# Optimization experiments

Measured on AMD Instinct MI355X. Metric: run time of the kernel, lower is better.

Reference implementation:

```python
import jax, jax.numpy as jnp
import numpy as np

EMBED = 1024
D_FF = 4 * EMBED
N_EXPERTS = 8
TOP_K = 2
B, S = 2, 1024


def setup_inputs() -> dict:
    key = jax.random.key(0)
    ks = jax.random.split(key, 10)
    sc_d = 1.0 / np.sqrt(EMBED)
    sc_h = 1.0 / np.sqrt(D_FF)
    return {
        "inputs": jax.random.normal(ks[0], (B, S, EMBED), jnp.float32),
        # router MLP: Linear(D,4D) -> ReLU -> Linear(4D,E)
        "rw1": jax.random.normal(ks[1], (EMBED, D_FF), jnp.float32) * sc_d,
        "rb1": jnp.zeros((D_FF,), jnp.float32),
        "rw2": jax.random.normal(ks[2], (D_FF, N_EXPERTS), jnp.float32) * sc_h,
        "rb2": jnp.zeros((N_EXPERTS,), jnp.float32),
        # stacked expert weights: Linear(D,4D) -> ReLU -> Linear(4D,D)
        "W1": jax.random.normal(ks[3], (N_EXPERTS, EMBED, D_FF), jnp.float32) * sc_d,
        "b1": jnp.zeros((N_EXPERTS, D_FF), jnp.float32),
        "W2": jax.random.normal(ks[4], (N_EXPERTS, D_FF, EMBED), jnp.float32) * sc_h,
        "b2": jnp.zeros((N_EXPERTS, EMBED), jnp.float32),
    }


def reference(inputs, rw1, rb1, rw2, rb2, W1, b1, W2, b2):
    Bb, Ss, D = inputs.shape
    T = Bb * Ss
    xf = inputs.reshape(T, D)  # [T, D]

    # Router: scores over experts, keep top-k, softmax over kept entries only.
    score = jax.nn.relu(xf @ rw1 + rb1) @ rw2 + rb2          # [T, E]
    _, topi = jax.lax.top_k(score, TOP_K)                    # [T, K]
    mask = jnp.zeros(score.shape, bool).at[jnp.arange(T)[:, None], topi].set(True)
    gate = jax.nn.softmax(jnp.where(mask, score, -jnp.inf), axis=-1)  # [T, E]

    # Dense per-expert MLP weighted by gate; gate==0 for non-top-k experts,
    # matching the original masked gather/scatter exactly.
    out = jnp.zeros_like(xf)
    for e in range(N_EXPERTS):
        h = jax.nn.relu(xf @ W1[e] + b1[e])                  # [T, 4D]
        y = h @ W2[e] + b2[e]                                # [T, D]
        out = out + gate[:, e:e + 1] * y
    return out.reshape(Bb, Ss, D)
```

## Files before the change

kernel.cpp:

```cpp
#include <hip/hip_runtime.h>
#include <stdint.h>

typedef unsigned short ushort_t;
typedef __attribute__((ext_vector_type(8))) short short8;
typedef __attribute__((ext_vector_type(4))) float f32x4;

#define EMBED   1024
#define DFF     4096
#define NEXP    8
#define TOKENS  2048
#define SLOTS   4096
#define TMAX    40

__device__ __forceinline__ ushort_t f2bf(float f) {
  unsigned u = __float_as_uint(f);
  u += 0x7FFFu + ((u >> 16) & 1u);
  return (ushort_t)(u >> 16);
}
__device__ __forceinline__ float bf2f(ushort_t b) {
  return __uint_as_float(((unsigned)b) << 16);
}

__device__ __forceinline__ void gl2lds16(const void* g, void* l) {
  typedef const __attribute__((address_space(1))) unsigned char* gp_t;
  typedef __attribute__((address_space(3))) unsigned char* lp_t;
  __builtin_amdgcn_global_load_lds((gp_t)(uintptr_t)g, (lp_t)(uintptr_t)l, 16, 0, 0);
}

__global__ void zero_small(int* counts, int* cursors) {
  int i = threadIdx.x;
  if (i < NEXP) { counts[i] = 0; cursors[i] = 0; }
}

__global__ void split_x3(const float* __restrict__ x, ushort_t* __restrict__ Xs) {
  int t = blockIdx.x;
  int d = threadIdx.x * 4;
  float4 v = *(const float4*)(x + (size_t)t * EMBED + d);
  ushort4 hi, lo;
  hi.x = f2bf(v.x); lo.x = f2bf(v.x - bf2f(hi.x));
  hi.y = f2bf(v.y); lo.y = f2bf(v.y - bf2f(hi.y));
  hi.z = f2bf(v.z); lo.z = f2bf(v.z - bf2f(hi.z));
  hi.w = f2bf(v.w); lo.w = f2bf(v.w - bf2f(hi.w));
  ushort_t* row = Xs + (size_t)t * 3072;
  *(ushort4*)(row + d)        = hi;
  *(ushort4*)(row + 1024 + d) = lo;
  *(ushort4*)(row + 2048 + d) = hi;
}

__global__ void transp_conv(const float* __restrict__ src, ushort_t* __restrict__ dst,
                            int src_ld, int dst_ld, long src_estride, long dst_estride,
                            int dst_koff, int lo)
{
  __shared__ float t[64][65];
  const float* s = src + (size_t)blockIdx.z * src_estride;
  ushort_t* d = dst + (size_t)blockIdx.z * dst_estride;
  int n0 = blockIdx.x * 64, k0 = blockIdx.y * 64;
  int tid = threadIdx.x;
  int kk = tid >> 4, nn = (tid & 15) * 4;
  #pragma unroll
  for (int it = 0; it < 4; it++) {
    float4 v = *(const float4*)(s + (size_t)(k0 + kk + it * 16) * src_ld + n0 + nn);
    t[kk + it * 16][nn]     = v.x;
    t[kk + it * 16][nn + 1] = v.y;
    t[kk + it * 16][nn + 2] = v.z;
    t[kk + it * 16][nn + 3] = v.w;
  }
  __syncthreads();
  int nn2 = tid >> 3, kk2 = (tid & 7) * 8;
  #pragma unroll
  for (int it = 0; it < 2; it++) {
    int n = nn2 + it * 32;
    union { ushort_t u[8]; uint4 v; } pk;
    #pragma unroll
    for (int j = 0; j < 8; j++) {
      float xv = t[kk2 + j][n];
      ushort_t hv = f2bf(xv);
      pk.u[j] = lo ? f2bf(xv - bf2f(hv)) : hv;
    }
    *(uint4*)(d + (size_t)(n0 + n) * dst_ld + dst_koff + k0 + kk2) = pk.v;
  }
}

template<int BPATH, int OUTMODE, bool RELU, bool EXPERT, int SPLITK, int NX>
__global__ __launch_bounds__(256, 4)
void gemm_kernel(const ushort_t* __restrict__ A, const void* __restrict__ Bv,
                 const float* __restrict__ bias, void* __restrict__ Cout,
                 const float* __restrict__ slot_gate,
                 const int* __restrict__ off, const int* __restrict__ tile_e,
                 const int* __restrict__ tile_y, int M, int N, int K)
{
  __shared__ ushort_t As[128 * 32];
  __shared__ ushort_t Bs[128 * 32];

  int e = 0, kc = 0, row0, col0, m_base, m_cnt;
  if (EXPERT) {
    int bid  = blockIdx.x;
    int xi   = bid % NX;
    int rest = bid / NX;
    kc       = rest % SPLITK;
    int t    = rest / SPLITK;
    e = tile_e[t];
    if (e < 0) return;
    row0   = tile_y[t] * 128;
    col0   = xi * 128;
    m_base = off[e];
    m_cnt  = off[e + 1] - m_base;
  } else {
    row0 = blockIdx.y * 128;
    col0 = blockIdx.x * 128;
    m_base = 0; m_cnt = M;
    if (row0 >= m_cnt) return;
  }
  const int Kc   = K / SPLITK;
  const int kbeg = kc * Kc;

  const int tid  = threadIdx.x;
  const int lane = tid & 63;
  const int wid  = tid >> 6;
  const int wm = wid & 1, wn = wid >> 1;

  const int srow  = lane >> 2;
  const int schk8 = ((lane & 3) ^ ((lane >> 3) & 3)) * 8;

  const ushort_t* gA[2];
  ushort_t *ldsA[2], *ldsB[2];
  #pragma unroll
  for (int h = 0; h < 2; h++) {
    int r  = row0 + h * 64 + wid * 16 + srow;
    int rg = m_base + min(r, m_cnt - 1);
    gA[h]   = A + (size_t)rg * K + kbeg + schk8;
    ldsA[h] = As + (h * 64 + wid * 16) * 32;
    ldsB[h] = Bs + (h * 64 + wid * 16) * 32;
  }
  const ushort_t* gB[2] = {nullptr, nullptr};
  const float* Bf = nullptr;
  if constexpr (BPATH == 0) {
    const ushort_t* Bt = (const ushort_t*)Bv + (EXPERT ? (size_t)e * N * K : 0);
    #pragma unroll
    for (int h = 0; h < 2; h++) {
      int n = col0 + h * 64 + wid * 16 + srow;
      gB[h] = Bt + (size_t)n * K + kbeg + schk8;
    }
  } else {
    Bf = (const float*)Bv + (EXPERT ? (size_t)e * (size_t)K * N : 0);
  }
  const int bn  = tid & 127;
  const int bc0 = (tid >> 7) << 1;

  f32x4 acc[4][4];
  #pragma unroll
  for (int i = 0; i < 4; i++)
    #pragma unroll
    for (int j = 0; j < 4; j++)
      acc[i][j] = (f32x4){0.f, 0.f, 0.f, 0.f};

  const int q  = lane >> 4;
  const int rr = lane & 15;
  const int sw8 = (q ^ ((rr >> 1) & 3)) * 8;
  const int abase = (wm * 64 + rr) * 32 + sw8;
  const int bbase = (wn * 64 + rr) * 32 + sw8;

  const int nkt = Kc >> 5;
  for (int kt = 0; kt < nkt; kt++) {
    const int k0 = kt << 5;
    __syncthreads();
    #pragma unroll
    for (int h = 0; h < 2; h++) gl2lds16(gA[h] + k0, ldsA[h]);
    if constexpr (BPATH == 0) {
      #pragma unroll
      for (int h = 0; h < 2; h++) gl2lds16(gB[h] + k0, ldsB[h]);
    } else {
      #pragma unroll
      for (int ci = 0; ci < 2; ci++) {
        int c = bc0 + ci;
        union { ushort_t u[8]; uint4 v; } pk;
        #pragma unroll
        for (int j = 0; j < 8; j++)
          pk.u[j] = f2bf(Bf[(size_t)(kbeg + k0 + c * 8 + j) * N + col0 + bn]);
        int s = c ^ ((bn >> 1) & 3);
        *(uint4*)(Bs + bn * 32 + s * 8) = pk.v;
      }
    }
    __syncthreads();

    short8 af[4], bfr[4];
    #pragma unroll
    for (int i = 0; i < 4; i++) {
      af[i]  = *(const short8*)(As + abase + i * 512);
      bfr[i] = *(const short8*)(Bs + bbase + i * 512);
    }
    #pragma unroll
    for (int mt = 0; mt < 4; mt++)
      #pragma unroll
      for (int nt = 0; nt < 4; nt++)
        acc[mt][nt] = __builtin_amdgcn_mfma_f32_16x16x32_bf16(af[mt], bfr[nt], acc[mt][nt], 0, 0, 0);
  }

  const float* biasp = bias + (EXPERT ? (size_t)e * N : 0);
  float bv[4];
  #pragma unroll
  for (int nt = 0; nt < 4; nt++)
    bv[nt] = biasp[col0 + wn * 64 + nt * 16 + rr];
  const float bscale = (SPLITK == 1 || kc == 0) ? 1.f : 0.f;

  #pragma unroll
  for (int mt = 0; mt < 4; mt++) {
    #pragma unroll
    for (int i = 0; i < 4; i++) {
      int r_loc = row0 + wm * 64 + mt * 16 + q * 4 + i;
      if (r_loc < m_cnt) {
        int slot = m_base + r_loc;
        float g = 1.f;
        if (OUTMODE == 3) g = slot_gate[slot];
        #pragma unroll
        for (int nt = 0; nt < 4; nt++) {
          float v = acc[mt][nt][i] + bscale * bv[nt];
          if (RELU) v = fmaxf(v, 0.f);
          int c = col0 + wn * 64 + nt * 16 + rr;
          if (OUTMODE == 0)      ((float*)Cout)[(size_t)slot * N + c]    = v;
          else if (OUTMODE == 1) ((ushort_t*)Cout)[(size_t)slot * N + c] = f2bf(v);
          else ((float*)Cout)[((size_t)kc * SLOTS + slot) * N + c] = g * v;
        }
      }
    }
  }
}

__global__ void router_score(const float* __restrict__ h, const float* __restrict__ rw2,
                             const float* __restrict__ rb2, int* __restrict__ topi,
                             float* __restrict__ gates, int* __restrict__ counts)
{
  int t = blockIdx.x * 4 + (threadIdx.x >> 6);
  if (t >= TOKENS) return;
  int lane = threadIdx.x & 63;
  const float* hr = h + (size_t)t * DFF;
  float acc[8] = {0,0,0,0,0,0,0,0};
  for (int j = lane; j < DFF; j += 64) {
    float hv = hr[j];
    const float4* w = (const float4*)(rw2 + (size_t)j * 8);
    float4 w0 = w[0], w1 = w[1];
    acc[0] += hv * w0.x; acc[1] += hv * w0.y; acc[2] += hv * w0.z; acc[3] += hv * w0.w;
    acc[4] += hv * w1.x; acc[5] += hv * w1.y; acc[6] += hv * w1.z; acc[7] += hv * w1.w;
  }
  #pragma unroll
  for (int e = 0; e < 8; e++)
    for (int o = 32; o > 0; o >>= 1)
      acc[e] += __shfl_down(acc[e], o);
  if (lane == 0) {
    float s[8];
    #pragma unroll
    for (int e = 0; e < 8; e++) s[e] = acc[e] + rb2[e];
    int i0 = 0;
    #pragma unroll
    for (int e = 1; e < 8; e++) if (s[e] > s[i0]) i0 = e;
    int i1 = (i0 == 0) ? 1 : 0;
    #pragma unroll
    for (int e = 0; e < 8; e++) if (e != i0 && s[e] > s[i1]) i1 = e;
    float ex = __expf(s[i1] - s[i0]);
    float g0 = 1.f / (1.f + ex);
    float g1 = ex / (1.f + ex);
    topi[t * 2] = i0; topi[t * 2 + 1] = i1;
    gates[t * 2] = g0; gates[t * 2 + 1] = g1;
    atomicAdd(&counts[i0], 1);
    atomicAdd(&counts[i1], 1);
  }
}

__global__ void prefix_off(const int* __restrict__ counts, int* __restrict__ off,
                           int* __restrict__ tile_e, int* __restrict__ tile_y)
{
  if (threadIdx.x == 0) {
    int a = 0, t = 0;
    for (int e = 0; e < NEXP; e++) {
      off[e] = a;
      int c = counts[e]; a += c;
      int ty = (c + 127) >> 7;
      for (int y = 0; y < ty; y++) { tile_e[t] = e; tile_y[t] = y; t++; }
    }
    off[NEXP] = a;
    for (; t < TMAX; t++) { tile_e[t] = -1; tile_y[t] = 0; }
  }
}

__global__ void assign_slots(const int* __restrict__ topi, const float* __restrict__ gates,
                             const int* __restrict__ off, int* __restrict__ cursors,
                             int* __restrict__ slot_token, float* __restrict__ slot_gate,
                             int* __restrict__ tok_slot)
{
  int t = blockIdx.x * blockDim.x + threadIdx.x;
  if (t >= TOKENS) return;
  #pragma unroll
  for (int k = 0; k < 2; k++) {
    int e = topi[t * 2 + k];
    int p = atomicAdd(&cursors[e], 1);
    int s = off[e] + p;
    slot_token[s] = t;
    slot_gate[s]  = gates[t * 2 + k];
    tok_slot[t * 2 + k] = s;
  }
}

__global__ void gather_x(const float* __restrict__ x, const int* __restrict__ slot_token,
                         ushort_t* __restrict__ Xg)
{
  int s = blockIdx.x;
  int t = slot_token[s];
  int d = threadIdx.x * 4;
  float4 v = *(const float4*)(x + (size_t)t * EMBED + d);
  ushort4 o;
  o.x = f2bf(v.x); o.y = f2bf(v.y); o.z = f2bf(v.z); o.w = f2bf(v.w);
  *(ushort4*)(Xg + (size_t)s * EMBED + d) = o;
}

__global__ void combine_out(const float* __restrict__ Ys, const int* __restrict__ tok_slot,
                            float* __restrict__ out)
{
  int t = blockIdx.x;
  int d = threadIdx.x * 4;
  int s0 = tok_slot[t * 2], s1 = tok_slot[t * 2 + 1];
  float4 a = *(const float4*)(Ys + (size_t)s0 * EMBED + d);
  float4 b = *(const float4*)(Ys + ((size_t)SLOTS + s0) * EMBED + d);
  float4 c = *(const float4*)(Ys + (size_t)s1 * EMBED + d);
  float4 e = *(const float4*)(Ys + ((size_t)SLOTS + s1) * EMBED + d);
  float4 o;
  o.x = (a.x + b.x) + (c.x + e.x);
  o.y = (a.y + b.y) + (c.y + e.y);
  o.z = (a.z + b.z) + (c.z + e.z);
  o.w = (a.w + b.w) + (c.w + e.w);
  *(float4*)(out + (size_t)t * EMBED + d) = o;
}

extern "C" void kernel_launch(void* const* d_in, const int* in_sizes, int n_in,
                              void* d_out, int out_size, void* d_ws, size_t ws_size,
                              hipStream_t stream)
{
  const float* x   = (const float*)d_in[0];
  const float* rw1 = (const float*)d_in[1];
  const float* rb1 = (const float*)d_in[2];
  const float* rw2 = (const float*)d_in[3];
  const float* rb2 = (const float*)d_in[4];
  const float* W1  = (const float*)d_in[5];
  const float* b1  = (const float*)d_in[6];
  const float* W2  = (const float*)d_in[7];
  const float* b2  = (const float*)d_in[8];
  float* out = (float*)d_out;
  char* ws = (char*)d_ws;

  const size_t SZ_RW1T = (size_t)4096 * 3072 * 2;
  const size_t SZ_XS3  = (size_t)2048 * 3072 * 2;
  const size_t SZ_XG   = (size_t)SLOTS * EMBED * 2;
  const size_t SZ_H    = (size_t)SLOTS * DFF * 2;

  ushort_t* RW1t = (ushort_t*)ws;
  float*    Ys   = (float*)ws;
  ushort_t* Xs3  = (ushort_t*)(ws + SZ_RW1T);
  ushort_t* Xg   = (ushort_t*)(ws + SZ_RW1T + SZ_XS3);
  ushort_t* Hs   = (ushort_t*)(ws + SZ_RW1T + SZ_XS3 + SZ_XG);
  float*    h    = (float*)Hs;
  char* ps = ws + SZ_RW1T + SZ_XS3 + SZ_XG + SZ_H;
  int*   topi       = (int*)ps;    ps += TOKENS * 2 * 4;
  float* gates      = (float*)ps;  ps += TOKENS * 2 * 4;
  int*   tok_slot   = (int*)ps;    ps += TOKENS * 2 * 4;
  int*   slot_token = (int*)ps;    ps += SLOTS * 4;
  float* slot_gate  = (float*)ps;  ps += SLOTS * 4;
  int*   counts     = (int*)ps;    ps += 256;
  int*   cursors    = (int*)ps;    ps += 256;
  int*   off        = (int*)ps;    ps += 256;
  int*   tile_e     = (int*)ps;    ps += 256;
  int*   tile_y     = (int*)ps;    ps += 256;

  zero_small<<<1, 64, 0, stream>>>(counts, cursors);
  split_x3<<<TOKENS, 256, 0, stream>>>(x, Xs3);

  transp_conv<<<dim3(64, 16, 1), 256, 0, stream>>>(rw1, RW1t, DFF, 3072, 0, 0, 0,    0);
  transp_conv<<<dim3(64, 16, 1), 256, 0, stream>>>(rw1, RW1t, DFF, 3072, 0, 0, 1024, 0);
  transp_conv<<<dim3(64, 16, 1), 256, 0, stream>>>(rw1, RW1t, DFF, 3072, 0, 0, 2048, 1);

  gemm_kernel<0, 0, true, false, 1, 32>
      <<<dim3(32, 16, 1), 256, 0, stream>>>(Xs3, RW1t, rb1, h, nullptr,
                                            nullptr, nullptr, nullptr, TOKENS, DFF, 3072);
  router_score<<<512, 256, 0, stream>>>(h, rw2, rb2, topi, gates, counts);
  prefix_off  <<<1, 64, 0, stream>>>(counts, off, tile_e, tile_y);
  assign_slots<<<8, 256, 0, stream>>>(topi, gates, off, cursors, slot_token, slot_gate, tok_slot);
  gather_x    <<<SLOTS, 256, 0, stream>>>(x, slot_token, Xg);

  gemm_kernel<1, 1, true, true, 1, 32>
      <<<dim3(32 * TMAX, 1, 1), 256, 0, stream>>>(Xg, W1, b1, Hs,
          nullptr, off, tile_e, tile_y, 0, DFF, EMBED);
  gemm_kernel<1, 3, false, true, 2, 8>
      <<<dim3(8 * 2 * TMAX, 1, 1), 256, 0, stream>>>(Hs, W2, b2, Ys,
          slot_gate, off, tile_e, tile_y, 0, EMBED, DFF);

  combine_out<<<TOKENS, 256, 0, stream>>>(Ys, tok_slot, out);
}
```

Before: 630.1 us.

## Double-buffer GEMM LDS tiles and fuse router weight split into GEMM loads

The GEMM main loop now double-buffers the A and B shared-memory tiles: it prefetches the next k-tile, holding fp32 B values in registers, while running MFMAs on the current one, so each iteration needs one barrier instead of two. It also drops the three transpose/convert kernels for the router weight. A new BPATH=2 mode reads rw1 directly in fp32 and builds the hi/hi/lo bf16 split on the fly from the k index. This removes three launches and a workspace round-trip, but doubles LDS use, lowers the occupancy hint from 4 to 3, and adds strided fp32 global loads to the router GEMM.

```diff
diff --git a/kernel.cpp b/kernel.cpp
--- a/kernel.cpp
+++ b/kernel.cpp
@@ -47,50 +47,16 @@
   *(ushort4*)(row + 2048 + d) = hi;
 }
 
-__global__ void transp_conv(const float* __restrict__ src, ushort_t* __restrict__ dst,
-                            int src_ld, int dst_ld, long src_estride, long dst_estride,
-                            int dst_koff, int lo)
-{
-  __shared__ float t[64][65];
-  const float* s = src + (size_t)blockIdx.z * src_estride;
-  ushort_t* d = dst + (size_t)blockIdx.z * dst_estride;
-  int n0 = blockIdx.x * 64, k0 = blockIdx.y * 64;
-  int tid = threadIdx.x;
-  int kk = tid >> 4, nn = (tid & 15) * 4;
-  #pragma unroll
-  for (int it = 0; it < 4; it++) {
-    float4 v = *(const float4*)(s + (size_t)(k0 + kk + it * 16) * src_ld + n0 + nn);
-    t[kk + it * 16][nn]     = v.x;
-    t[kk + it * 16][nn + 1] = v.y;
-    t[kk + it * 16][nn + 2] = v.z;
-    t[kk + it * 16][nn + 3] = v.w;
-  }
-  __syncthreads();
-  int nn2 = tid >> 3, kk2 = (tid & 7) * 8;
-  #pragma unroll
-  for (int it = 0; it < 2; it++) {
-    int n = nn2 + it * 32;
-    union { ushort_t u[8]; uint4 v; } pk;
-    #pragma unroll
-    for (int j = 0; j < 8; j++) {
-      float xv = t[kk2 + j][n];
-      ushort_t hv = f2bf(xv);
-      pk.u[j] = lo ? f2bf(xv - bf2f(hv)) : hv;
-    }
-    *(uint4*)(d + (size_t)(n0 + n) * dst_ld + dst_koff + k0 + kk2) = pk.v;
-  }
-}
-
 template<int BPATH, int OUTMODE, bool RELU, bool EXPERT, int SPLITK, int NX>
-__global__ __launch_bounds__(256, 4)
+__global__ __launch_bounds__(256, 3)
 void gemm_kernel(const ushort_t* __restrict__ A, const void* __restrict__ Bv,
                  const float* __restrict__ bias, void* __restrict__ Cout,
                  const float* __restrict__ slot_gate,
                  const int* __restrict__ off, const int* __restrict__ tile_e,
                  const int* __restrict__ tile_y, int M, int N, int K)
 {
-  __shared__ ushort_t As[128 * 32];
-  __shared__ ushort_t Bs[128 * 32];
+  __shared__ ushort_t As[2][128 * 32];
+  __shared__ ushort_t Bs[2][128 * 32];
 
   int e = 0, kc = 0, row0, col0, m_base, m_cnt;
   if (EXPERT) {
@@ -123,14 +89,13 @@
   const int schk8 = ((lane & 3) ^ ((lane >> 3) & 3)) * 8;
 
   const ushort_t* gA[2];
-  ushort_t *ldsA[2], *ldsB[2];
+  int aoff[2];
   #pragma unroll
   for (int h = 0; h < 2; h++) {
     int r  = row0 + h * 64 + wid * 16 + srow;
     int rg = m_base + min(r, m_cnt - 1);
     gA[h]   = A + (size_t)rg * K + kbeg + schk8;
-    ldsA[h] = As + (h * 64 + wid * 16) * 32;
-    ldsB[h] = Bs + (h * 64 + wid * 16) * 32;
+    aoff[h] = (h * 64 + wid * 16) * 32;
   }
   const ushort_t* gB[2] = {nullptr, nullptr};
   const float* Bf = nullptr;
@@ -146,6 +111,43 @@
   }
   const int bn  = tid & 127;
   const int bc0 = (tid >> 7) << 1;
+
+  auto stageA = [&](int pb, int k0) {
+    #pragma unroll
+    for (int h = 0; h < 2; h++)
+      gl2lds16(gA[h] + k0, &As[pb][aoff[h]]);
+  };
+  auto stageBdma = [&](int pb, int k0) {
+    #pragma unroll
+    for (int h = 0; h < 2; h++)
+      gl2lds16(gB[h] + k0, &Bs[pb][aoff[h]]);
+  };
+  auto issueB = [&](int k0, float* br) {
+    #pragma unroll
+    for (int ci = 0; ci < 2; ci++)
+      #pragma unroll
+      for (int j = 0; j < 8; j++) {
+        int kk = kbeg + k0 + (bc0 + ci) * 8 + j;
+        int krow = (BPATH == 2) ? ((kk < 2048) ? (kk & 1023) : (kk - 2048)) : kk;
+        br[ci * 8 + j] = Bf[(size_t)krow * N + col0 + bn];
+      }
+  };
+  auto writeB = [&](int pb, int k0, const float* br) {
+    #pragma unroll
+    for (int ci = 0; ci < 2; ci++) {
+      int c = bc0 + ci;
+      bool lo = (BPATH == 2) && ((kbeg + k0 + c * 8) >= 2048);
+      union { ushort_t u[8]; uint4 v; } pk;
+      #pragma unroll
+      for (int j = 0; j < 8; j++) {
+        float xv = br[ci * 8 + j];
+        ushort_t hv = f2bf(xv);
+        pk.u[j] = lo ? f2bf(xv - bf2f(hv)) : hv;
+      }
+      int s = c ^ ((bn >> 1) & 3);
+      *(uint4*)(&Bs[pb][bn * 32 + s * 8]) = pk.v;
+    }
+  };
 
   f32x4 acc[4][4];
   #pragma unroll
@@ -161,39 +163,42 @@
   const int bbase = (wn * 64 + rr) * 32 + sw8;
 
   const int nkt = Kc >> 5;
+
+  stageA(0, 0);
+  if constexpr (BPATH == 0) {
+    stageBdma(0, 0);
+  } else {
+    float br0[16];
+    issueB(0, br0);
+    writeB(0, 0, br0);
+  }
+  __syncthreads();
+
   for (int kt = 0; kt < nkt; kt++) {
-    const int k0 = kt << 5;
-    __syncthreads();
-    #pragma unroll
-    for (int h = 0; h < 2; h++) gl2lds16(gA[h] + k0, ldsA[h]);
-    if constexpr (BPATH == 0) {
-      #pragma unroll
-      for (int h = 0; h < 2; h++) gl2lds16(gB[h] + k0, ldsB[h]);
-    } else {
-      #pragma unroll
-      for (int ci = 0; ci < 2; ci++) {
-        int c = bc0 + ci;
-        union { ushort_t u[8]; uint4 v; } pk;
-        #pragma unroll
-        for (int j = 0; j < 8; j++)
-          pk.u[j] = f2bf(Bf[(size_t)(kbeg + k0 + c * 8 + j) * N + col0 + bn]);
-        int s = c ^ ((bn >> 1) & 3);
-        *(uint4*)(Bs + bn * 32 + s * 8) = pk.v;
-      }
-    }
-    __syncthreads();
+    const int cur = kt & 1, nxt = cur ^ 1;
+    const int k0n = (kt + 1) << 5;
+    const bool hn = (kt + 1 < nkt);
+    float breg[16];
+    if (hn) {
+      stageA(nxt, k0n);
+      if constexpr (BPATH == 0) stageBdma(nxt, k0n);
+      else issueB(k0n, breg);
+    }
 
     short8 af[4], bfr[4];
     #pragma unroll
     for (int i = 0; i < 4; i++) {
-      af[i]  = *(const short8*)(As + abase + i * 512);
-      bfr[i] = *(const short8*)(Bs + bbase + i * 512);
+      af[i]  = *(const short8*)(&As[cur][abase + i * 512]);
+      bfr[i] = *(const short8*)(&Bs[cur][bbase + i * 512]);
     }
     #pragma unroll
     for (int mt = 0; mt < 4; mt++)
       #pragma unroll
       for (int nt = 0; nt < 4; nt++)
         acc[mt][nt] = __builtin_amdgcn_mfma_f32_16x16x32_bf16(af[mt], bfr[nt], acc[mt][nt], 0, 0, 0);
+
+    if (hn && BPATH >= 1) writeB(nxt, k0n, breg);
+    __syncthreads();
   }
 
   const float* biasp = bias + (EXPERT ? (size_t)e * N : 0);
@@ -351,7 +356,6 @@
   const size_t SZ_XG   = (size_t)SLOTS * EMBED * 2;
   const size_t SZ_H    = (size_t)SLOTS * DFF * 2;
 
-  ushort_t* RW1t = (ushort_t*)ws;
   float*    Ys   = (float*)ws;
   ushort_t* Xs3  = (ushort_t*)(ws + SZ_RW1T);
   ushort_t* Xg   = (ushort_t*)(ws + SZ_RW1T + SZ_XS3);
@@ -372,12 +376,8 @@
   zero_small<<<1, 64, 0, stream>>>(counts, cursors);
   split_x3<<<TOKENS, 256, 0, stream>>>(x, Xs3);
 
-  transp_conv<<<dim3(64, 16, 1), 256, 0, stream>>>(rw1, RW1t, DFF, 3072, 0, 0, 0,    0);
-  transp_conv<<<dim3(64, 16, 1), 256, 0, stream>>>(rw1, RW1t, DFF, 3072, 0, 0, 1024, 0);
-  transp_conv<<<dim3(64, 16, 1), 256, 0, stream>>>(rw1, RW1t, DFF, 3072, 0, 0, 2048, 1);
-
-  gemm_kernel<0, 0, true, false, 1, 32>
-      <<<dim3(32, 16, 1), 256, 0, stream>>>(Xs3, RW1t, rb1, h, nullptr,
+  gemm_kernel<2, 0, true, false, 1, 32>
+      <<<dim3(32, 16, 1), 256, 0, stream>>>(Xs3, rw1, rb1, h, nullptr,
                                             nullptr, nullptr, nullptr, TOKENS, DFF, 3072);
   router_score<<<512, 256, 0, stream>>>(h, rw2, rb2, topi, gates, counts);
   prefix_off  <<<1, 64, 0, stream>>>(counts, off, tile_e, tile_y);
```

Result: slower. 665.9 us (+5.7%).

## Pre-transpose expert weights to bf16, double-buffer LDS, gather tokens inside GEMM

Applied to the files above, without the earlier changes.

Expert W1/W2 are now transposed and converted to bf16 in batches of four experts into a shared workspace. The expert GEMMs then load B with async global-to-LDS copies instead of per-element fp32 loads and conversion. The GEMM gains a double-buffered LDS pipeline that prefetches the next K tile during MFMA work. The A operand is indexed directly from the hi/lo split of x (and via slot_token for the expert GEMM), which removes the gather_x kernel and the duplicated hi copy. This adds extra transpose passes over all expert weights and more kernel launches, and lowers occupancy to 3 blocks per CU.

```diff
diff --git a/kernel.cpp b/kernel.cpp
--- a/kernel.cpp
+++ b/kernel.cpp
@@ -32,7 +32,7 @@
   if (i < NEXP) { counts[i] = 0; cursors[i] = 0; }
 }
 
-__global__ void split_x3(const float* __restrict__ x, ushort_t* __restrict__ Xs) {
+__global__ void split_xhl(const float* __restrict__ x, ushort_t* __restrict__ Xs) {
   int t = blockIdx.x;
   int d = threadIdx.x * 4;
   float4 v = *(const float4*)(x + (size_t)t * EMBED + d);
@@ -41,10 +41,9 @@
   hi.y = f2bf(v.y); lo.y = f2bf(v.y - bf2f(hi.y));
   hi.z = f2bf(v.z); lo.z = f2bf(v.z - bf2f(hi.z));
   hi.w = f2bf(v.w); lo.w = f2bf(v.w - bf2f(hi.w));
-  ushort_t* row = Xs + (size_t)t * 3072;
+  ushort_t* row = Xs + (size_t)t * 2048;
   *(ushort4*)(row + d)        = hi;
   *(ushort4*)(row + 1024 + d) = lo;
-  *(ushort4*)(row + 2048 + d) = hi;
 }
 
 __global__ void transp_conv(const float* __restrict__ src, ushort_t* __restrict__ dst,
@@ -81,16 +80,17 @@
   }
 }
 
-template<int BPATH, int OUTMODE, bool RELU, bool EXPERT, int SPLITK, int NX>
-__global__ __launch_bounds__(256, 4)
-void gemm_kernel(const ushort_t* __restrict__ A, const void* __restrict__ Bv,
+template<int APATH, int OUTMODE, bool RELU, bool EXPERT, int SPLITK, int NX>
+__global__ __launch_bounds__(256, 3)
+void gemm_kernel(const ushort_t* __restrict__ A, const ushort_t* __restrict__ B,
                  const float* __restrict__ bias, void* __restrict__ Cout,
-                 const float* __restrict__ slot_gate,
+                 const float* __restrict__ slot_gate, const int* __restrict__ slot_token,
                  const int* __restrict__ off, const int* __restrict__ tile_e,
-                 const int* __restrict__ tile_y, int M, int N, int K)
-{
-  __shared__ ushort_t As[128 * 32];
-  __shared__ ushort_t Bs[128 * 32];
+                 const int* __restrict__ tile_y, int e0, int e1,
+                 int M, int N, int K)
+{
+  __shared__ ushort_t As[2][128 * 32];
+  __shared__ ushort_t Bs[2][128 * 32];
 
   int e = 0, kc = 0, row0, col0, m_base, m_cnt;
   if (EXPERT) {
@@ -100,7 +100,7 @@
     kc       = rest % SPLITK;
     int t    = rest / SPLITK;
     e = tile_e[t];
-    if (e < 0) return;
+    if (e < e0 || e >= e1) return;
     row0   = tile_y[t] * 128;
     col0   = xi * 128;
     m_base = off[e];
@@ -123,29 +123,32 @@
   const int schk8 = ((lane & 3) ^ ((lane >> 3) & 3)) * 8;
 
   const ushort_t* gA[2];
-  ushort_t *ldsA[2], *ldsB[2];
+  const ushort_t* gB[2];
+  int aoff[2];
+  const ushort_t* Bt = B + (EXPERT ? (size_t)(e - e0) * (size_t)N * K : 0);
   #pragma unroll
   for (int h = 0; h < 2; h++) {
     int r  = row0 + h * 64 + wid * 16 + srow;
-    int rg = m_base + min(r, m_cnt - 1);
-    gA[h]   = A + (size_t)rg * K + kbeg + schk8;
-    ldsA[h] = As + (h * 64 + wid * 16) * 32;
-    ldsB[h] = Bs + (h * 64 + wid * 16) * 32;
-  }
-  const ushort_t* gB[2] = {nullptr, nullptr};
-  const float* Bf = nullptr;
-  if constexpr (BPATH == 0) {
-    const ushort_t* Bt = (const ushort_t*)Bv + (EXPERT ? (size_t)e * N * K : 0);
+    int rl = min(r, m_cnt - 1);
+    size_t rowb;
+    if (APATH == 2)      rowb = (size_t)slot_token[m_base + rl] * 2048;
+    else if (APATH == 1) rowb = (size_t)rl * 2048;
+    else                 rowb = (size_t)(m_base + rl) * (size_t)K;
+    gA[h]   = A + rowb + (APATH == 0 ? kbeg : 0) + schk8;
+    aoff[h] = (h * 64 + wid * 16) * 32;
+
+    int n = col0 + h * 64 + wid * 16 + srow;
+    gB[h] = Bt + (size_t)n * K + kbeg + schk8;
+  }
+
+  auto stage = [&](int pb, int k0) {
+    const int k0a = (APATH == 1 && k0 >= 2048) ? k0 - 2048 : k0;
     #pragma unroll
     for (int h = 0; h < 2; h++) {
-      int n = col0 + h * 64 + wid * 16 + srow;
-      gB[h] = Bt + (size_t)n * K + kbeg + schk8;
-    }
-  } else {
-    Bf = (const float*)Bv + (EXPERT ? (size_t)e * (size_t)K * N : 0);
-  }
-  const int bn  = tid & 127;
-  const int bc0 = (tid >> 7) << 1;
+      gl2lds16(gA[h] + k0a, &As[pb][aoff[h]]);
+      gl2lds16(gB[h] + k0,  &Bs[pb][aoff[h]]);
+    }
+  };
 
   f32x4 acc[4][4];
   #pragma unroll
@@ -161,39 +164,27 @@
   const int bbase = (wn * 64 + rr) * 32 + sw8;
 
   const int nkt = Kc >> 5;
+
+  stage(0, 0);
+  __syncthreads();
+
   for (int kt = 0; kt < nkt; kt++) {
-    const int k0 = kt << 5;
-    __syncthreads();
-    #pragma unroll
-    for (int h = 0; h < 2; h++) gl2lds16(gA[h] + k0, ldsA[h]);
-    if constexpr (BPATH == 0) {
-      #pragma unroll
-      for (int h = 0; h < 2; h++) gl2lds16(gB[h] + k0, ldsB[h]);
-    } else {
-      #pragma unroll
-      for (int ci = 0; ci < 2; ci++) {
-        int c = bc0 + ci;
-        union { ushort_t u[8]; uint4 v; } pk;
-        #pragma unroll
-        for (int j = 0; j < 8; j++)
-          pk.u[j] = f2bf(Bf[(size_t)(kbeg + k0 + c * 8 + j) * N + col0 + bn]);
-        int s = c ^ ((bn >> 1) & 3);
-        *(uint4*)(Bs + bn * 32 + s * 8) = pk.v;
-      }
-    }
-    __syncthreads();
+    const int cur = kt & 1, nxt = cur ^ 1;
+    if (kt + 1 < nkt) stage(nxt, (kt + 1) << 5);
 
     short8 af[4], bfr[4];
     #pragma unroll
     for (int i = 0; i < 4; i++) {
-      af[i]  = *(const short8*)(As + abase + i * 512);
-      bfr[i] = *(const short8*)(Bs + bbase + i * 512);
+      af[i]  = *(const short8*)(&As[cur][abase + i * 512]);
+      bfr[i] = *(const short8*)(&Bs[cur][bbase + i * 512]);
     }
     #pragma unroll
     for (int mt = 0; mt < 4; mt++)
       #pragma unroll
       for (int nt = 0; nt < 4; nt++)
         acc[mt][nt] = __builtin_amdgcn_mfma_f32_16x16x32_bf16(af[mt], bfr[nt], acc[mt][nt], 0, 0, 0);
+
+    __syncthreads();
   }
 
   const float* biasp = bias + (EXPERT ? (size_t)e * N : 0);
@@ -300,18 +291,6 @@
   }
 }
 
-__global__ void gather_x(const float* __restrict__ x, const int* __restrict__ slot_token,
-                         ushort_t* __restrict__ Xg)
-{
-  int s = blockIdx.x;
-  int t = slot_token[s];
-  int d = threadIdx.x * 4;
-  float4 v = *(const float4*)(x + (size_t)t * EMBED + d);
-  ushort4 o;
-  o.x = f2bf(v.x); o.y = f2bf(v.y); o.z = f2bf(v.z); o.w = f2bf(v.w);
-  *(ushort4*)(Xg + (size_t)s * EMBED + d) = o;
-}
-
 __global__ void combine_out(const float* __restrict__ Ys, const int* __restrict__ tok_slot,
                             float* __restrict__ out)
 {
@@ -346,18 +325,15 @@
   float* out = (float*)d_out;
   char* ws = (char*)d_ws;
 
-  const size_t SZ_RW1T = (size_t)4096 * 3072 * 2;
-  const size_t SZ_XS3  = (size_t)2048 * 3072 * 2;
-  const size_t SZ_XG   = (size_t)SLOTS * EMBED * 2;
-  const size_t SZ_H    = (size_t)SLOTS * DFF * 2;
+  const size_t SZ_R = (size_t)4096 * 4096 * 2;
 
   ushort_t* RW1t = (ushort_t*)ws;
-  float*    Ys   = (float*)ws;
-  ushort_t* Xs3  = (ushort_t*)(ws + SZ_RW1T);
-  ushort_t* Xg   = (ushort_t*)(ws + SZ_RW1T + SZ_XS3);
-  ushort_t* Hs   = (ushort_t*)(ws + SZ_RW1T + SZ_XS3 + SZ_XG);
-  float*    h    = (float*)Hs;
-  char* ps = ws + SZ_RW1T + SZ_XS3 + SZ_XG + SZ_H;
+  ushort_t* WT   = (ushort_t*)ws;
+  float*    h    = (float*)(ws + SZ_R);
+  ushort_t* Hs   = (ushort_t*)(ws + SZ_R);
+  ushort_t* Xhl  = (ushort_t*)(ws + 2 * SZ_R);
+  float*    Ys   = (float*)(ws + 2 * SZ_R);
+  char* ps = ws + 3 * SZ_R;
   int*   topi       = (int*)ps;    ps += TOKENS * 2 * 4;
   float* gates      = (float*)ps;  ps += TOKENS * 2 * 4;
   int*   tok_slot   = (int*)ps;    ps += TOKENS * 2 * 4;
@@ -370,26 +346,39 @@
   int*   tile_y     = (int*)ps;    ps += 256;
 
   zero_small<<<1, 64, 0, stream>>>(counts, cursors);
-  split_x3<<<TOKENS, 256, 0, stream>>>(x, Xs3);
+  split_xhl<<<TOKENS, 256, 0, stream>>>(x, Xhl);
 
   transp_conv<<<dim3(64, 16, 1), 256, 0, stream>>>(rw1, RW1t, DFF, 3072, 0, 0, 0,    0);
   transp_conv<<<dim3(64, 16, 1), 256, 0, stream>>>(rw1, RW1t, DFF, 3072, 0, 0, 1024, 0);
   transp_conv<<<dim3(64, 16, 1), 256, 0, stream>>>(rw1, RW1t, DFF, 3072, 0, 0, 2048, 1);
 
-  gemm_kernel<0, 0, true, false, 1, 32>
-      <<<dim3(32, 16, 1), 256, 0, stream>>>(Xs3, RW1t, rb1, h, nullptr,
-                                            nullptr, nullptr, nullptr, TOKENS, DFF, 3072);
+  gemm_kernel<1, 0, true, false, 1, 32>
+      <<<dim3(32, 16, 1), 256, 0, stream>>>(Xhl, RW1t, rb1, h, nullptr, nullptr,
+                                            nullptr, nullptr, nullptr, 0, NEXP,
+                                            TOKENS, DFF, 3072);
   router_score<<<512, 256, 0, stream>>>(h, rw2, rb2, topi, gates, counts);
   prefix_off  <<<1, 64, 0, stream>>>(counts, off, tile_e, tile_y);
   assign_slots<<<8, 256, 0, stream>>>(topi, gates, off, cursors, slot_token, slot_gate, tok_slot);
-  gather_x    <<<SLOTS, 256, 0, stream>>>(x, slot_token, Xg);
-
-  gemm_kernel<1, 1, true, true, 1, 32>
-      <<<dim3(32 * TMAX, 1, 1), 256, 0, stream>>>(Xg, W1, b1, Hs,
-          nullptr, off, tile_e, tile_y, 0, DFF, EMBED);
-  gemm_kernel<1, 3, false, true, 2, 8>
-      <<<dim3(8 * 2 * TMAX, 1, 1), 256, 0, stream>>>(Hs, W2, b2, Ys,
-          slot_gate, off, tile_e, tile_y, 0, EMBED, DFF);
+
+  const long W1ES = (long)EMBED * DFF;
+  const long W2ES = (long)DFF * EMBED;
+
+  for (int half = 0; half < 2; half++) {
+    int e0 = half * 4;
+    transp_conv<<<dim3(64, 16, 4), 256, 0, stream>>>(W1 + (size_t)e0 * W1ES, WT,
+        DFF, EMBED, W1ES, W1ES, 0, 0);
+    gemm_kernel<2, 1, true, true, 1, 32>
+        <<<dim3(32 * TMAX, 1, 1), 256, 0, stream>>>(Xhl, WT, b1, Hs,
+            nullptr, slot_token, off, tile_e, tile_y, e0, e0 + 4, 0, DFF, EMBED);
+  }
+  for (int half = 0; half < 2; half++) {
+    int e0 = half * 4;
+    transp_conv<<<dim3(16, 64, 4), 256, 0, stream>>>(W2 + (size_t)e0 * W2ES, WT,
+        EMBED, DFF, W2ES, W2ES, 0, 0);
+    gemm_kernel<0, 3, false, true, 2, 8>
+        <<<dim3(8 * 2 * TMAX, 1, 1), 256, 0, stream>>>(Hs, WT, b2, Ys,
+            slot_gate, nullptr, off, tile_e, tile_y, e0, e0 + 4, 0, EMBED, DFF);
+  }
 
   combine_out<<<TOKENS, 256, 0, stream>>>(Ys, tok_slot, out);
 }
```

Result: slower. 646.1 us (+2.5%).
